# Kernel tuning notes

Measured on AMD Instinct MI355X. Metric: run time of the kernel, lower is better.

Reference implementation:

```python
import jax, jax.numpy as jnp
import numpy as np

NUM_GROUPS = 32
EPS = 1e-5
HEAD_DIM = 64

def group_norm(x, w, b):
    # x: [B,C,H,W]; normalize within 32 groups over (C//32, H, W)
    B, C, H, W = x.shape
    xg = x.reshape(B, NUM_GROUPS, C // NUM_GROUPS, H, W)
    mu = xg.mean(axis=(2, 3, 4), keepdims=True)
    var = xg.var(axis=(2, 3, 4), keepdims=True)
    xn = ((xg - mu) / jnp.sqrt(var + EPS)).reshape(B, C, H, W)
    return xn * w[None, :, None, None] + b[None, :, None, None]

def conv1x1(x, w, b):
    # w: [Cout, Cin], b: [Cout]
    return jnp.einsum('bchw,oc->bohw', x, w) + b[None, :, None, None]

def setup_inputs() -> dict:
    key = jax.random.key(0)
    ks = jax.random.split(key, 12)
    B, C, Cc, H, W = 16, 512, 512, 32, 32
    s = 0.02
    return {
        'x': jax.random.normal(ks[0], (B, C, H, W), jnp.float32),
        'context': jax.random.normal(ks[1], (B, Cc, H, W), jnp.float32),
        'norm_q_w': jnp.ones((C,), jnp.float32),
        'norm_q_b': jnp.zeros((C,), jnp.float32),
        'norm_kv_w': jnp.ones((Cc,), jnp.float32),
        'norm_kv_b': jnp.zeros((Cc,), jnp.float32),
        'conv_q_w': jax.random.normal(ks[2], (C, C), jnp.float32) * s,
        'conv_q_b': jnp.zeros((C,), jnp.float32),
        'conv_kv_w': jax.random.normal(ks[3], (2 * C, Cc), jnp.float32) * s,
        'conv_kv_b': jnp.zeros((2 * C,), jnp.float32),
        'proj_w': jax.random.normal(ks[4], (C, C), jnp.float32) * s,
        'proj_b': jnp.zeros((C,), jnp.float32),
    }

def reference(x, context, norm_q_w, norm_q_b, norm_kv_w, norm_kv_b,
              conv_q_w, conv_q_b, conv_kv_w, conv_kv_b, proj_w, proj_b):
    B, C, H, W = x.shape
    nh = max(1, C // HEAD_DIM)
    hd = C // nh
    q = conv1x1(group_norm(x, norm_q_w, norm_q_b), conv_q_w, conv_q_b)
    kv = conv1x1(group_norm(context, norm_kv_w, norm_kv_b), conv_kv_w, conv_kv_b)
    k, v = jnp.split(kv, 2, axis=1)
    L = H * W
    q = q.reshape(B, nh, hd, L)
    k = k.reshape(B, nh, hd, L)
    v = v.reshape(B, nh, hd, L)
    attn = jnp.einsum('bhdi,bhdj->bhij', q, k) * (hd ** -0.5)
    attn = jax.nn.softmax(attn, axis=-1)
    out = jnp.einsum('bhij,bhdj->bhdi', attn, v)
    return x + conv1x1(out.reshape(B, C, H, W), proj_w, proj_b)
```

## Files before the change

kernel.cpp:

```cpp
#include <hip/hip_runtime.h>
#include <hip/hip_bf16.h>

typedef short v8s __attribute__((ext_vector_type(8)));
typedef float v4f __attribute__((ext_vector_type(4)));
typedef float v16f __attribute__((ext_vector_type(16)));
typedef __hip_bfloat16 bf16;

__device__ __forceinline__ float b2f(bf16 h) { return __bfloat162float(h); }
__device__ __forceinline__ bf16 f2b(float f) { return __float2bfloat16(f); }

#define QSCALE 0.18033688f

__device__ __forceinline__ void gll16(const void* g, void* l) {
    __builtin_amdgcn_global_load_lds(
        (const __attribute__((address_space(1))) void*)g,
        (__attribute__((address_space(3))) void*)l, 16, 0, 0);
}

__device__ __forceinline__ unsigned cvtpk(float lo, float hi_) {
    unsigned r;
    asm("v_cvt_pk_bf16_f32 %0, %1, %2" : "=v"(r) : "v"(lo), "v"(hi_));
    return r;
}

__device__ __forceinline__ void pl32swap(unsigned& a, unsigned& b) {
    asm("v_permlane32_swap_b32 %0, %1" : "+v"(a), "+v"(b));
}

__global__ __launch_bounds__(256) void gn_t_kernel(
    const float* __restrict__ x, const float* __restrict__ ctx,
    const float* __restrict__ qw, const float* __restrict__ qb,
    const float* __restrict__ kw, const float* __restrict__ kb,
    bf16* __restrict__ xnT, bf16* __restrict__ cnT)
{
    const int b = blockIdx.y, g = blockIdx.x, z = blockIdx.z, c0 = g * 16;
    const float* src = z ? ctx : x;
    const float* gw  = z ? kw : qw;
    const float* gb  = z ? kb : qb;
    bf16* dst = z ? cnT : xnT;
    __shared__ __attribute__((aligned(16))) bf16 lx[16][1032];
    __shared__ float rS[4], rQ[4];
    __shared__ float sSc[16], sSh[16];
    const int t = threadIdx.x, wave = t >> 6, lane = t & 63;
    const float* xb = src + ((long)b * 512 + c0) * 1024;
    float sum = 0.f, sq = 0.f;
#pragma unroll
    for (int i = 0; i < 16; i++) {
        int q = t + i * 256;
        int ci = q >> 8, l0 = (q & 255) * 4;
        float4 v = *(const float4*)(xb + (long)ci * 1024 + l0);
        sum += v.x + v.y + v.z + v.w;
        sq  += v.x * v.x + v.y * v.y + v.z * v.z + v.w * v.w;
        union { short4 s4v; bf16 h[4]; } w;
        w.h[0] = f2b(v.x); w.h[1] = f2b(v.y); w.h[2] = f2b(v.z); w.h[3] = f2b(v.w);
        *(short4*)&lx[ci][l0] = w.s4v;
    }
#pragma unroll
    for (int off = 32; off > 0; off >>= 1) {
        sum += __shfl_down(sum, off);
        sq  += __shfl_down(sq, off);
    }
    if (lane == 0) { rS[wave] = sum; rQ[wave] = sq; }
    __syncthreads();
    if (t < 16) {
        float S = rS[0] + rS[1] + rS[2] + rS[3];
        float Q = rQ[0] + rQ[1] + rQ[2] + rQ[3];
        const float inv_n = 1.f / 16384.f;
        float mean = S * inv_n;
        float var  = Q * inv_n - mean * mean;
        float rstd = rsqrtf(var + 1e-5f);
        float w = gw[c0 + t];
        sSc[t] = rstd * w;
        sSh[t] = gb[c0 + t] - mean * rstd * w;
    }
    __syncthreads();
#pragma unroll
    for (int i = 0; i < 8; i++) {
        int p = t + i * 256;
        int l = p >> 1, half = (p & 1) * 8;
        union { float4 f4; bf16 h[8]; } o_;
#pragma unroll
        for (int j = 0; j < 8; j++) {
            float y = b2f(lx[half + j][l]) * sSc[half + j] + sSh[half + j];
            o_.h[j] = f2b(y);
        }
        *(float4*)(dst + ((long)b * 1024 + l) * 512 + c0 + half) = o_.f4;
    }
}

__global__ __launch_bounds__(256) void wconv_kernel(
    const float* __restrict__ a, const float* __restrict__ bsrc,
    const float* __restrict__ csrc, bf16* __restrict__ oa,
    bf16* __restrict__ ob, bf16* __restrict__ oc)
{
    int id = blockIdx.x * 256 + threadIdx.x;
    const float* src; bf16* dst; int off;
    if (id < 65536)       { src = a;    dst = oa; off = id; }
    else if (id < 196608) { src = bsrc; dst = ob; off = id - 65536; }
    else                  { src = csrc; dst = oc; off = id - 196608; }
    float4 v = ((const float4*)src)[off];
    union { short4 s4v; bf16 h[4]; } w;
    w.h[0] = f2b(v.x); w.h[1] = f2b(v.y); w.h[2] = f2b(v.z); w.h[3] = f2b(v.w);
    ((short4*)dst)[off] = w.s4v;
}

__global__ __launch_bounds__(256) void qkv_gemm_kernel(
    const bf16* __restrict__ xnT, const bf16* __restrict__ cnT,
    const bf16* __restrict__ wQ, const bf16* __restrict__ wKV,
    bf16* __restrict__ QT, bf16* __restrict__ KT, bf16* __restrict__ Vo,
    const float* __restrict__ cqb, const float* __restrict__ ckvb)
{
    const long PB = 512L * 1024;
    const int z = blockIdx.z, op = z >> 4, bz = z & 15;
    const bf16* A; const bf16* B; bf16* C; const float* bias;
    int nBlkN, N, biasPerM; float scale;
    if (op == 0) {
        A = xnT + bz * PB; B = wQ;  C = QT + bz * PB; bias = cqb;
        nBlkN = 4; N = 512; biasPerM = 0; scale = QSCALE;
    } else if (op == 1) {
        A = cnT + bz * PB; B = wKV; C = KT + bz * PB; bias = ckvb;
        nBlkN = 4; N = 512; biasPerM = 0; scale = 1.0f;
    } else {
        A = wKV + 512L * 512; B = cnT + bz * PB; C = Vo + bz * PB; bias = ckvb + 512;
        nBlkN = 8; N = 1024; biasPerM = 1; scale = 1.0f;
    }
    const int bx = blockIdx.x;
    const int m0 = (bx / nBlkN) * 128, n0 = (bx % nBlkN) * 128;
    __shared__ __attribute__((aligned(16))) bf16 lA[128][64];
    __shared__ __attribute__((aligned(16))) bf16 lB[128][64];
    const int t = threadIdx.x, wave = t >> 6, lane = t & 63;
    const int quad = lane >> 4, c = lane & 15;
    const int wm = (wave >> 1) * 64, wn = (wave & 1) * 64;
    const int rIS = lane >> 3;
    const int chG = (lane & 7) ^ rIS;
    const bf16* Ag[4]; const bf16* Bg[4];
    bf16* Al[4]; bf16* Bl[4];
#pragma unroll
    for (int j = 0; j < 4; j++) {
        int seg = wave + j * 4;
        int row = seg * 8 + rIS;
        Ag[j] = A + (long)(m0 + row) * 512 + chG * 8;
        Bg[j] = B + (long)(n0 + row) * 512 + chG * 8;
        Al[j] = &lA[seg * 8][0];
        Bl[j] = &lB[seg * 8][0];
    }
    v4f acc[4][4] = {};
    for (int k0 = 0; k0 < 512; k0 += 64) {
        __syncthreads();
#pragma unroll
        for (int j = 0; j < 4; j++) {
            gll16(Ag[j] + k0, Al[j]);
            gll16(Bg[j] + k0, Bl[j]);
        }
        __syncthreads();
#pragma unroll
        for (int kk = 0; kk < 2; kk++) {
            v8s af[4], bfr[4];
#pragma unroll
            for (int mt = 0; mt < 4; mt++)
                af[mt] = *(const v8s*)&lA[wm + mt * 16 + c][((kk * 4 + quad) ^ (c & 7)) * 8];
#pragma unroll
            for (int nt = 0; nt < 4; nt++)
                bfr[nt] = *(const v8s*)&lB[wn + nt * 16 + c][((kk * 4 + quad) ^ (c & 7)) * 8];
#pragma unroll
            for (int mt = 0; mt < 4; mt++)
#pragma unroll
                for (int nt = 0; nt < 4; nt++)
                    acc[mt][nt] = __builtin_amdgcn_mfma_f32_16x16x32_bf16(
                        af[mt], bfr[nt], acc[mt][nt], 0, 0, 0);
        }
    }
#pragma unroll
    for (int mt = 0; mt < 4; mt++) {
#pragma unroll
        for (int nt = 0; nt < 4; nt++) {
#pragma unroll
            for (int r = 0; r < 4; r++) {
                int row = m0 + wm + mt * 16 + quad * 4 + r;
                int col = n0 + wn + nt * 16 + c;
                float v = (acc[mt][nt][r] + (biasPerM ? bias[row] : bias[col])) * scale;
                C[(long)row * N + col] = f2b(v);
            }
        }
    }
}

__global__ __launch_bounds__(256) void gemm_proj_kernel(
    const bf16* __restrict__ A,
    const bf16* __restrict__ B, long sBb,
    float* __restrict__ C,
    const float* __restrict__ bias,
    const float* __restrict__ resid,
    int M, int N)
{
    const int bz = blockIdx.z;
    const int m0 = blockIdx.x * 128, n0 = blockIdx.y * 128;
    const bf16* Bb = B + (long)bz * sBb;
    __shared__ __attribute__((aligned(16))) bf16 lA[128][64];
    __shared__ __attribute__((aligned(16))) bf16 lB[128][64];
    const int t = threadIdx.x, wave = t >> 6, lane = t & 63;
    const int quad = lane >> 4, c = lane & 15;
    const int wm = (wave >> 1) * 64, wn = (wave & 1) * 64;
    const int rIS = lane >> 3, chG = (lane & 7) ^ rIS;
    const bf16* Ag[4]; const bf16* Bg[4];
    bf16* Al[4]; bf16* Bl[4];
#pragma unroll
    for (int j = 0; j < 4; j++) {
        int seg = wave + j * 4;
        int row = seg * 8 + rIS;
        Ag[j] = A + (long)(m0 + row) * 512 + chG * 8;
        Bg[j] = Bb + (long)(n0 + row) * 512 + chG * 8;
        Al[j] = &lA[seg * 8][0];
        Bl[j] = &lB[seg * 8][0];
    }
    v4f acc[4][4] = {};
    for (int k0 = 0; k0 < 512; k0 += 64) {
        __syncthreads();
#pragma unroll
        for (int j = 0; j < 4; j++) {
            gll16(Ag[j] + k0, Al[j]);
            gll16(Bg[j] + k0, Bl[j]);
        }
        __syncthreads();
#pragma unroll
        for (int kk = 0; kk < 2; kk++) {
            v8s af[4], bfr[4];
#pragma unroll
            for (int mt = 0; mt < 4; mt++)
                af[mt] = *(const v8s*)&lA[wm + mt * 16 + c][((kk * 4 + quad) ^ (c & 7)) * 8];
#pragma unroll
            for (int nt = 0; nt < 4; nt++)
                bfr[nt] = *(const v8s*)&lB[wn + nt * 16 + c][((kk * 4 + quad) ^ (c & 7)) * 8];
#pragma unroll
            for (int mt = 0; mt < 4; mt++)
#pragma unroll
                for (int nt = 0; nt < 4; nt++)
                    acc[mt][nt] = __builtin_amdgcn_mfma_f32_16x16x32_bf16(
                        af[mt], bfr[nt], acc[mt][nt], 0, 0, 0);
        }
    }
#pragma unroll
    for (int mt = 0; mt < 4; mt++) {
#pragma unroll
        for (int nt = 0; nt < 4; nt++) {
#pragma unroll
            for (int r = 0; r < 4; r++) {
                int row = m0 + wm + mt * 16 + quad * 4 + r;
                int col = n0 + wn + nt * 16 + c;
                float v = acc[mt][nt][r] + bias[row]
                        + resid[(long)bz * ((long)M * N) + (long)row * N + col];
                C[(long)bz * ((long)M * N) + (long)row * N + col] = v;
            }
        }
    }
}

__global__ __launch_bounds__(256, 2) void attn_kernel(
    const bf16* QT, const bf16* __restrict__ KT,
    const bf16* __restrict__ V, bf16* AOT)
{
    const int nblk = blockIdx.x;
    const int s = nblk >> 3;
    const int it = s & 3;
    const int g = ((s >> 2) << 3) | (nblk & 7);
    const int h = g & 7, b = g >> 3;
    const int i0 = it * 256;
    __shared__ __attribute__((aligned(16))) bf16 lk[2][64][64];
    __shared__ __attribute__((aligned(16))) bf16 lv[2][64][64];
    const int t = threadIdx.x, wave = t >> 6, lane = t & 63;
    const int m31 = lane & 31, hi = lane >> 5;
    const int rIS = lane >> 3, chG = (lane & 7) ^ rIS;
    v8s qf[2][4];
#pragma unroll
    for (int iq = 0; iq < 2; iq++) {
        const bf16* Qb = QT + ((long)b * 1024 + i0 + wave * 64 + iq * 32 + m31) * 512 + h * 64;
#pragma unroll
        for (int ks = 0; ks < 4; ks++)
            qf[iq][ks] = *(const v8s*)(Qb + ks * 16 + hi * 8);
    }
    const bf16* Kg[2]; const bf16* Vg[2];
#pragma unroll
    for (int j = 0; j < 2; j++) {
        int seg = wave * 2 + j;
        Kg[j] = KT + ((long)b * 1024 + seg * 8 + rIS) * 512 + h * 64 + chG * 8;
        Vg[j] = V + ((long)b * 512 + h * 64 + seg * 8 + rIS) * 1024 + chG * 8;
    }
#pragma unroll
    for (int j = 0; j < 2; j++) {
        int seg = wave * 2 + j;
        gll16(Kg[j], &lk[0][seg * 8][0]);
        gll16(Vg[j], &lv[0][seg * 8][0]);
    }
    float lsum[2] = {};
    v16f o[2][2] = {};

    for (int jt = 0; jt < 16; jt++) {
        const int cur = jt & 1;
        __syncthreads();
        {
            int nx = (jt + 1) & 15;
#pragma unroll
            for (int j = 0; j < 2; j++) {
                int seg = wave * 2 + j;
                gll16(Kg[j] + (long)nx * 64 * 512, &lk[1 - cur][seg * 8][0]);
                gll16(Vg[j] + (long)nx * 64, &lv[1 - cur][seg * 8][0]);
            }
        }
#pragma unroll
        for (int jb = 0; jb < 2; jb++) {
            v16f sA0 = {}, sA1 = {};
#pragma unroll
            for (int ks = 0; ks < 4; ks++) {
                v8s kf = *(const v8s*)&lk[cur][jb * 32 + m31][((ks * 2 + hi) ^ (m31 & 7)) * 8];
                sA0 = __builtin_amdgcn_mfma_f32_32x32x16_bf16(kf, qf[0][ks], sA0, 0, 0, 0);
                sA1 = __builtin_amdgcn_mfma_f32_32x32x16_bf16(kf, qf[1][ks], sA1, 0, 0, 0);
            }
            unsigned u0[8], u1[8];
#pragma unroll
            for (int k2 = 0; k2 < 8; k2++) {
                float p0l = exp2f(sA0[2 * k2]);
                float p0h = exp2f(sA0[2 * k2 + 1]);
                float p1l = exp2f(sA1[2 * k2]);
                float p1h = exp2f(sA1[2 * k2 + 1]);
                lsum[0] += p0l + p0h;
                lsum[1] += p1l + p1h;
                u0[k2] = cvtpk(p0l, p0h);
                u1[k2] = cvtpk(p1l, p1h);
            }
            pl32swap(u0[0], u0[2]); pl32swap(u0[1], u0[3]);
            pl32swap(u0[4], u0[6]); pl32swap(u0[5], u0[7]);
            pl32swap(u1[0], u1[2]); pl32swap(u1[1], u1[3]);
            pl32swap(u1[4], u1[6]); pl32swap(u1[5], u1[7]);
#pragma unroll
            for (int kk = 0; kk < 2; kk++) {
                union { unsigned w[4]; v8s v; } pf0, pf1;
                pf0.w[0] = u0[4 * kk + 0]; pf0.w[1] = u0[4 * kk + 1];
                pf0.w[2] = u0[4 * kk + 2]; pf0.w[3] = u0[4 * kk + 3];
                pf1.w[0] = u1[4 * kk + 0]; pf1.w[1] = u1[4 * kk + 1];
                pf1.w[2] = u1[4 * kk + 2]; pf1.w[3] = u1[4 * kk + 3];
                const int cc2 = (jb * 2 + kk) * 2 + hi;
                v8s vf0 = *(const v8s*)&lv[cur][m31][(cc2 ^ (m31 & 7)) * 8];
                o[0][0] = __builtin_amdgcn_mfma_f32_32x32x16_bf16(vf0, pf0.v, o[0][0], 0, 0, 0);
                o[1][0] = __builtin_amdgcn_mfma_f32_32x32x16_bf16(vf0, pf1.v, o[1][0], 0, 0, 0);
                v8s vf1 = *(const v8s*)&lv[cur][32 + m31][(cc2 ^ (m31 & 7)) * 8];
                o[0][1] = __builtin_amdgcn_mfma_f32_32x32x16_bf16(vf1, pf0.v, o[0][1], 0, 0, 0);
                o[1][1] = __builtin_amdgcn_mfma_f32_32x32x16_bf16(vf1, pf1.v, o[1][1], 0, 0, 0);
            }
        }
    }
#pragma unroll
    for (int iq = 0; iq < 2; iq++) {
        float lt = lsum[iq] + __shfl_xor(lsum[iq], 32);
        float inv = 1.f / lt;
        bf16* Ob = AOT + ((long)b * 1024 + i0 + wave * 64 + iq * 32 + m31) * 512 + h * 64;
#pragma unroll
        for (int gq = 0; gq < 4; gq++) {
            union { short4 s4v; bf16 hh[4]; } w0, w1;
#pragma unroll
            for (int k = 0; k < 4; k++) {
                w0.hh[k] = f2b(o[iq][0][gq * 4 + k] * inv);
                w1.hh[k] = f2b(o[iq][1][gq * 4 + k] * inv);
            }
            *(short4*)(Ob + gq * 8 + hi * 4)      = w0.s4v;
            *(short4*)(Ob + 32 + gq * 8 + hi * 4) = w1.s4v;
        }
    }
}

extern "C" void kernel_launch(void* const* d_in, const int* in_sizes, int n_in,
                              void* d_out, int out_size, void* d_ws, size_t ws_size,
                              hipStream_t stream)
{
    const float* x    = (const float*)d_in[0];
    const float* ctx  = (const float*)d_in[1];
    const float* nqw  = (const float*)d_in[2];
    const float* nqb  = (const float*)d_in[3];
    const float* nkw  = (const float*)d_in[4];
    const float* nkb  = (const float*)d_in[5];
    const float* cqw  = (const float*)d_in[6];
    const float* cqb  = (const float*)d_in[7];
    const float* ckvw = (const float*)d_in[8];
    const float* ckvb = (const float*)d_in[9];
    const float* pw   = (const float*)d_in[10];
    const float* pb   = (const float*)d_in[11];
    float* out = (float*)d_out;
    bf16* ws  = (bf16*)d_ws;

    const long PB  = 512L * 1024;
    const long TOT = 16L * PB;
    bf16* s0 = ws;
    bf16* s1 = ws + TOT;
    bf16* s2 = ws + 2 * TOT;
    bf16* s3 = ws + 3 * TOT;
    bf16* s4 = ws + 4 * TOT;
    bf16* wQ  = ws + 5 * TOT;
    bf16* wKV = wQ + 262144;
    bf16* wP  = wKV + 524288;

    dim3 blk(256);
    gn_t_kernel<<<dim3(32, 16, 2), blk, 0, stream>>>(
        x, ctx, nqw, nqb, nkw, nkb, s0, s1);
    wconv_kernel<<<dim3(1024), blk, 0, stream>>>(cqw, ckvw, pw, wQ, wKV, wP);
    qkv_gemm_kernel<<<dim3(32, 1, 48), blk, 0, stream>>>(
        s0, s1, wQ, wKV, s2, s3, s4, cqb, ckvb);
    attn_kernel<<<dim3(512), blk, 0, stream>>>(s2, s3, s4, s2);
    gemm_proj_kernel<<<dim3(4, 8, 16), blk, 0, stream>>>(
        wP, s2, PB, out, pb, x, 512, 1024);
}
```

Baseline: 255.9 us.

## Triple-buffer K/V tiles in attention with explicit vmcnt wait and MFMA priority

Moves the attention kernel's K/V LDS staging from double to triple buffering, prefetching two tiles ahead. The full __syncthreads is replaced by a partial vmcnt wait plus a raw s_barrier, so loads can stay in flight across iterations. It also computes both score blocks before the softmax, raises wave priority around the MFMA sections, and uses the hardware exp2 intrinsic. In exchange it uses more LDS per block, which could limit occupancy, and relies on a hand-tuned vmcnt count being correct.

```diff
diff --git a/kernel.cpp b/kernel.cpp
--- a/kernel.cpp
+++ b/kernel.cpp
@@ -265,8 +265,8 @@
     const int g = ((s >> 2) << 3) | (nblk & 7);
     const int h = g & 7, b = g >> 3;
     const int i0 = it * 256;
-    __shared__ __attribute__((aligned(16))) bf16 lk[2][64][64];
-    __shared__ __attribute__((aligned(16))) bf16 lv[2][64][64];
+    __shared__ __attribute__((aligned(16))) bf16 lk[3][64][64];
+    __shared__ __attribute__((aligned(16))) bf16 lv[3][64][64];
     const int t = threadIdx.x, wave = t >> 6, lane = t & 63;
     const int m31 = lane & 31, hi = lane >> 5;
     const int rIS = lane >> 3, chG = (lane & 7) ^ rIS;
@@ -285,84 +285,98 @@
         Kg[j] = KT + ((long)b * 1024 + seg * 8 + rIS) * 512 + h * 64 + chG * 8;
         Vg[j] = V + ((long)b * 512 + h * 64 + seg * 8 + rIS) * 1024 + chG * 8;
     }
-#pragma unroll
-    for (int j = 0; j < 2; j++) {
-        int seg = wave * 2 + j;
-        gll16(Kg[j], &lk[0][seg * 8][0]);
-        gll16(Vg[j], &lv[0][seg * 8][0]);
-    }
-    float lsum[2] = {};
-    v16f o[2][2] = {};
+    auto issue = [&](int jtx, int bi) {
+#pragma unroll
+        for (int j = 0; j < 2; j++) {
+            int seg = wave * 2 + j;
+            gll16(Kg[j] + (long)jtx * 64 * 512, &lk[bi][seg * 8][0]);
+            gll16(Vg[j] + (long)jtx * 64,      &lv[bi][seg * 8][0]);
+        }
+    };
+    issue(0, 0);
+    issue(1, 1);
+    float lsum0 = 0.f, lsum1 = 0.f;
+    v16f o00 = {}, o01 = {}, o10 = {}, o11 = {};
+
+#define SMPV(sj0, sj1, JB)                                                     \
+    {                                                                          \
+        unsigned u0[8], u1[8];                                                 \
+        _Pragma("unroll")                                                      \
+        for (int k2 = 0; k2 < 8; k2++) {                                       \
+            float p0l = __builtin_amdgcn_exp2f(sj0[2 * k2]);                   \
+            float p0h = __builtin_amdgcn_exp2f(sj0[2 * k2 + 1]);               \
+            float p1l = __builtin_amdgcn_exp2f(sj1[2 * k2]);                   \
+            float p1h = __builtin_amdgcn_exp2f(sj1[2 * k2 + 1]);               \
+            lsum0 += p0l + p0h; lsum1 += p1l + p1h;                            \
+            u0[k2] = cvtpk(p0l, p0h); u1[k2] = cvtpk(p1l, p1h);                \
+        }                                                                      \
+        pl32swap(u0[0], u0[2]); pl32swap(u0[1], u0[3]);                        \
+        pl32swap(u0[4], u0[6]); pl32swap(u0[5], u0[7]);                        \
+        pl32swap(u1[0], u1[2]); pl32swap(u1[1], u1[3]);                        \
+        pl32swap(u1[4], u1[6]); pl32swap(u1[5], u1[7]);                        \
+        __builtin_amdgcn_s_setprio(1);                                         \
+        _Pragma("unroll")                                                      \
+        for (int kk = 0; kk < 2; kk++) {                                       \
+            union { unsigned w[4]; v8s v; } pf0, pf1;                          \
+            pf0.w[0] = u0[4 * kk + 0]; pf0.w[1] = u0[4 * kk + 1];              \
+            pf0.w[2] = u0[4 * kk + 2]; pf0.w[3] = u0[4 * kk + 3];              \
+            pf1.w[0] = u1[4 * kk + 0]; pf1.w[1] = u1[4 * kk + 1];              \
+            pf1.w[2] = u1[4 * kk + 2]; pf1.w[3] = u1[4 * kk + 3];              \
+            const int cc2 = ((JB) * 2 + kk) * 2 + hi;                          \
+            v8s vf0 = *(const v8s*)&lv[cur][m31][(cc2 ^ (m31 & 7)) * 8];       \
+            o00 = __builtin_amdgcn_mfma_f32_32x32x16_bf16(vf0, pf0.v, o00, 0, 0, 0); \
+            o10 = __builtin_amdgcn_mfma_f32_32x32x16_bf16(vf0, pf1.v, o10, 0, 0, 0); \
+            v8s vf1 = *(const v8s*)&lv[cur][32 + m31][(cc2 ^ (m31 & 7)) * 8];  \
+            o01 = __builtin_amdgcn_mfma_f32_32x32x16_bf16(vf1, pf0.v, o01, 0, 0, 0); \
+            o11 = __builtin_amdgcn_mfma_f32_32x32x16_bf16(vf1, pf1.v, o11, 0, 0, 0); \
+        }                                                                      \
+        __builtin_amdgcn_s_setprio(0);                                         \
+    }
 
     for (int jt = 0; jt < 16; jt++) {
-        const int cur = jt & 1;
-        __syncthreads();
-        {
-            int nx = (jt + 1) & 15;
-#pragma unroll
-            for (int j = 0; j < 2; j++) {
-                int seg = wave * 2 + j;
-                gll16(Kg[j] + (long)nx * 64 * 512, &lk[1 - cur][seg * 8][0]);
-                gll16(Vg[j] + (long)nx * 64, &lv[1 - cur][seg * 8][0]);
+        const int cur = jt % 3;
+        asm volatile("s_waitcnt vmcnt(4)" ::: "memory");
+        __builtin_amdgcn_s_barrier();
+        __builtin_amdgcn_sched_barrier(0);
+        issue((jt + 2) & 15, (jt + 2) % 3);
+        v16f s00 = {}, s01 = {}, s10 = {}, s11 = {};
+        __builtin_amdgcn_s_setprio(1);
+#pragma unroll
+        for (int ks = 0; ks < 4; ks++) {
+            const int chs = ((ks * 2 + hi) ^ (m31 & 7)) * 8;
+            v8s kf0 = *(const v8s*)&lk[cur][m31][chs];
+            v8s kf1 = *(const v8s*)&lk[cur][32 + m31][chs];
+            s00 = __builtin_amdgcn_mfma_f32_32x32x16_bf16(kf0, qf[0][ks], s00, 0, 0, 0);
+            s01 = __builtin_amdgcn_mfma_f32_32x32x16_bf16(kf0, qf[1][ks], s01, 0, 0, 0);
+            s10 = __builtin_amdgcn_mfma_f32_32x32x16_bf16(kf1, qf[0][ks], s10, 0, 0, 0);
+            s11 = __builtin_amdgcn_mfma_f32_32x32x16_bf16(kf1, qf[1][ks], s11, 0, 0, 0);
+        }
+        __builtin_amdgcn_s_setprio(0);
+        SMPV(s00, s01, 0)
+        SMPV(s10, s11, 1)
+    }
+#undef SMPV
+    {
+        float lt0 = lsum0 + __shfl_xor(lsum0, 32);
+        float lt1 = lsum1 + __shfl_xor(lsum1, 32);
+        float inv0 = 1.f / lt0, inv1 = 1.f / lt1;
+#pragma unroll
+        for (int iq = 0; iq < 2; iq++) {
+            float inv = iq ? inv1 : inv0;
+            const v16f& oa = iq ? o10 : o00;
+            const v16f& ob = iq ? o11 : o01;
+            bf16* Ob = AOT + ((long)b * 1024 + i0 + wave * 64 + iq * 32 + m31) * 512 + h * 64;
+#pragma unroll
+            for (int gq = 0; gq < 4; gq++) {
+                union { short4 s4v; bf16 hh[4]; } w0, w1;
+#pragma unroll
+                for (int k = 0; k < 4; k++) {
+                    w0.hh[k] = f2b(oa[gq * 4 + k] * inv);
+                    w1.hh[k] = f2b(ob[gq * 4 + k] * inv);
+                }
+                *(short4*)(Ob + gq * 8 + hi * 4)      = w0.s4v;
+                *(short4*)(Ob + 32 + gq * 8 + hi * 4) = w1.s4v;
             }
-        }
-#pragma unroll
-        for (int jb = 0; jb < 2; jb++) {
-            v16f sA0 = {}, sA1 = {};
-#pragma unroll
-            for (int ks = 0; ks < 4; ks++) {
-                v8s kf = *(const v8s*)&lk[cur][jb * 32 + m31][((ks * 2 + hi) ^ (m31 & 7)) * 8];
-                sA0 = __builtin_amdgcn_mfma_f32_32x32x16_bf16(kf, qf[0][ks], sA0, 0, 0, 0);
-                sA1 = __builtin_amdgcn_mfma_f32_32x32x16_bf16(kf, qf[1][ks], sA1, 0, 0, 0);
-            }
-            unsigned u0[8], u1[8];
-#pragma unroll
-            for (int k2 = 0; k2 < 8; k2++) {
-                float p0l = exp2f(sA0[2 * k2]);
-                float p0h = exp2f(sA0[2 * k2 + 1]);
-                float p1l = exp2f(sA1[2 * k2]);
-                float p1h = exp2f(sA1[2 * k2 + 1]);
-                lsum[0] += p0l + p0h;
-                lsum[1] += p1l + p1h;
-                u0[k2] = cvtpk(p0l, p0h);
-                u1[k2] = cvtpk(p1l, p1h);
-            }
-            pl32swap(u0[0], u0[2]); pl32swap(u0[1], u0[3]);
-            pl32swap(u0[4], u0[6]); pl32swap(u0[5], u0[7]);
-            pl32swap(u1[0], u1[2]); pl32swap(u1[1], u1[3]);
-            pl32swap(u1[4], u1[6]); pl32swap(u1[5], u1[7]);
-#pragma unroll
-            for (int kk = 0; kk < 2; kk++) {
-                union { unsigned w[4]; v8s v; } pf0, pf1;
-                pf0.w[0] = u0[4 * kk + 0]; pf0.w[1] = u0[4 * kk + 1];
-                pf0.w[2] = u0[4 * kk + 2]; pf0.w[3] = u0[4 * kk + 3];
-                pf1.w[0] = u1[4 * kk + 0]; pf1.w[1] = u1[4 * kk + 1];
-                pf1.w[2] = u1[4 * kk + 2]; pf1.w[3] = u1[4 * kk + 3];
-                const int cc2 = (jb * 2 + kk) * 2 + hi;
-                v8s vf0 = *(const v8s*)&lv[cur][m31][(cc2 ^ (m31 & 7)) * 8];
-                o[0][0] = __builtin_amdgcn_mfma_f32_32x32x16_bf16(vf0, pf0.v, o[0][0], 0, 0, 0);
-                o[1][0] = __builtin_amdgcn_mfma_f32_32x32x16_bf16(vf0, pf1.v, o[1][0], 0, 0, 0);
-                v8s vf1 = *(const v8s*)&lv[cur][32 + m31][(cc2 ^ (m31 & 7)) * 8];
-                o[0][1] = __builtin_amdgcn_mfma_f32_32x32x16_bf16(vf1, pf0.v, o[0][1], 0, 0, 0);
-                o[1][1] = __builtin_amdgcn_mfma_f32_32x32x16_bf16(vf1, pf1.v, o[1][1], 0, 0, 0);
-            }
-        }
-    }
-#pragma unroll
-    for (int iq = 0; iq < 2; iq++) {
-        float lt = lsum[iq] + __shfl_xor(lsum[iq], 32);
-        float inv = 1.f / lt;
-        bf16* Ob = AOT + ((long)b * 1024 + i0 + wave * 64 + iq * 32 + m31) * 512 + h * 64;
-#pragma unroll
-        for (int gq = 0; gq < 4; gq++) {
-            union { short4 s4v; bf16 hh[4]; } w0, w1;
-#pragma unroll
-            for (int k = 0; k < 4; k++) {
-                w0.hh[k] = f2b(o[iq][0][gq * 4 + k] * inv);
-                w1.hh[k] = f2b(o[iq][1][gq * 4 + k] * inv);
-            }
-            *(short4*)(Ob + gq * 8 + hi * 4)      = w0.s4v;
-            *(short4*)(Ob + 32 + gq * 8 + hi * 4) = w1.s4v;
         }
     }
 }
```

Result: faster. 237.5 us (-7.2%).
